# Performance work log

Hardware: AMD Instinct MI355X
Metric: run time of the kernel (lower is better)

Reference implementation:

```python
import jax, jax.numpy as jnp
import numpy as np

N_EMBD = 1024
N_HEAD = 16
HEAD_DIM = N_EMBD // N_HEAD


def setup_inputs() -> dict:
    key = jax.random.key(0)
    ks = jax.random.split(key, 8)
    B, T, T_ctx, C = 2, 2048, 2048, N_EMBD
    s = 1.0 / np.sqrt(C)
    return {
        "x": jax.random.normal(ks[0], (B, T, C), dtype=jnp.float32),
        "context": jax.random.normal(ks[1], (B, T_ctx, C), dtype=jnp.float32),
        # Linear weights stored as [in, out] (torch stores [out, in]; math identical via x @ W)
        "Wq": jax.random.normal(ks[2], (C, C), dtype=jnp.float32) * s,
        "bq": jnp.zeros((C,), dtype=jnp.float32),
        "Wkv": jax.random.normal(ks[3], (C, 2 * C), dtype=jnp.float32) * s,
        "bkv": jnp.zeros((2 * C,), dtype=jnp.float32),
        "Wp": jax.random.normal(ks[4], (C, C), dtype=jnp.float32) * s,
        "bp": jnp.zeros((C,), dtype=jnp.float32),
    }


def reference(x, context, Wq, bq, Wkv, bkv, Wp, bp):
    B, T, C = x.shape
    T_ctx = context.shape[1]
    H, D = N_HEAD, C // N_HEAD

    q = (x @ Wq + bq).reshape(B, T, H, D).transpose(0, 2, 1, 3)          # [B,H,T,D]
    kv = context @ Wkv + bkv                                             # [B,T_ctx,2C]
    k, v = jnp.split(kv, 2, axis=-1)
    k = k.reshape(B, T_ctx, H, D).transpose(0, 2, 1, 3)                  # [B,H,T_ctx,D]
    v = v.reshape(B, T_ctx, H, D).transpose(0, 2, 1, 3)                  # [B,H,T_ctx,D]

    att = jnp.einsum("bhtd,bhsd->bhts", q, k) * (1.0 / jnp.sqrt(jnp.asarray(D, q.dtype)))
    # tril(ones(T, T_ctx)): position t attends to context positions s <= t
    causal = jnp.arange(T)[:, None] >= jnp.arange(T_ctx)[None, :]        # [T,T_ctx]
    att = jnp.where(causal[None, None], att, jnp.asarray(-jnp.inf, att.dtype))
    att = jax.nn.softmax(att, axis=-1)

    y = jnp.einsum("bhts,bhsd->bhtd", att, v)                            # [B,H,T,D]
    y = y.transpose(0, 2, 1, 3).reshape(B, T, C)
    return y @ Wp + bp
```

## Files before the change

### kernel.cpp

```cpp
#include <hip/hip_runtime.h>
#include <hip/hip_bf16.h>

typedef __bf16 bf16;
typedef __bf16 bf16x8 __attribute__((ext_vector_type(8)));
typedef __bf16 bf16x4 __attribute__((ext_vector_type(4)));
typedef float f32x4 __attribute__((ext_vector_type(4)));
typedef float f32x16 __attribute__((ext_vector_type(16)));

#define GLOAD_LDS16(g, l) \
  __builtin_amdgcn_global_load_lds((const __attribute__((address_space(1))) void*)(g), \
                                   (__attribute__((address_space(3))) void*)(l), 16, 0, 0)

static __device__ __forceinline__ unsigned cvtpk_bf16(float lo, float hi) {
  unsigned r;
  asm("v_cvt_pk_bf16_f32 %0, %1, %2" : "=v"(r) : "v"(lo), "v"(hi));
  return r;
}
static __device__ __forceinline__ void pl32swap(unsigned& a, unsigned& b) {
  asm volatile("v_permlane32_swap_b32 %0, %1" : "+v"(a), "+v"(b));
}

__global__ __launch_bounds__(256) void prep_kernel(
    const float* __restrict__ x, const float* __restrict__ ctx,
    const float* __restrict__ Wq, const float* __restrict__ Wkv, const float* __restrict__ Wp,
    bf16* __restrict__ x_bf, bf16* __restrict__ c_bf,
    bf16* __restrict__ Wq_t, bf16* __restrict__ Wkv_t, bf16* __restrict__ Wp_t) {
  const int bid = blockIdx.x;
  if (bid < 8192) {
    const int i = (bid & 4095) * 256 + threadIdx.x;
    const float4 v = (bid < 4096) ? ((const float4*)x)[i] : ((const float4*)ctx)[i];
    bf16x4 o;
    o.x = (bf16)v.x; o.y = (bf16)v.y; o.z = (bf16)v.z; o.w = (bf16)v.w;
    if (bid < 4096) ((bf16x4*)x_bf)[i] = o; else ((bf16x4*)c_bf)[i] = o;
    return;
  }
  __shared__ float tile[32][33];
  int tb = bid - 8192;
  const float* W; bf16* Wt; int N;
  if (tb < 1024) { W = Wq; Wt = Wq_t; N = 1024; }
  else if (tb < 3072) { W = Wkv; Wt = Wkv_t; N = 2048; tb -= 1024; }
  else { W = Wp; Wt = Wp_t; N = 1024; tb -= 3072; }
  const int nt = N >> 5;
  const int n0 = (tb % nt) * 32, k0 = (tb / nt) * 32;
  const int tx = threadIdx.x & 31, ty = threadIdx.x >> 5;
#pragma unroll
  for (int i = 0; i < 32; i += 8)
    tile[ty + i][tx] = W[(size_t)(k0 + ty + i) * N + n0 + tx];
  __syncthreads();
#pragma unroll
  for (int i = 0; i < 32; i += 8)
    Wt[(size_t)(n0 + ty + i) * 1024 + k0 + tx] = (bf16)tile[tx][ty + i];
}

__global__ __launch_bounds__(512) void proj_gemm_kernel(
    const bf16* __restrict__ x_bf, const bf16* __restrict__ c_bf,
    const bf16* __restrict__ Wq_t, const bf16* __restrict__ Wkv_t,
    const float* __restrict__ bq, const float* __restrict__ bkv,
    bf16* __restrict__ Qh, bf16* __restrict__ Kh, bf16* __restrict__ Vt) {
  __shared__ __align__(16) bf16 SM[24576];
  bf16* As = SM;
  bf16* Bs = SM + 16384;
  bf16* Vb = SM;

  const int tid = threadIdx.x;
  const int lane = tid & 63;
  const int w = tid >> 6;
  const int wm = w >> 2, wn = w & 3;
  const int g4 = lane >> 4, r16 = lane & 15;
  const int wu = __builtin_amdgcn_readfirstlane(w);

  int bid = blockIdx.x;
  bid = (bid & 7) * 48 + (bid >> 3);
  const bool isq = bid < 128;
  const int lid = isq ? bid : bid - 128;
  const int bx = isq ? (lid & 7) : (lid & 15);
  const int by = isq ? (lid >> 3) : (lid >> 4);
  const int m0 = by * 256, n0 = bx * 128;
  const bf16* A = isq ? x_bf : c_bf;
  const bf16* Bt = isq ? Wq_t : Wkv_t;
  const float* bias = isq ? bq : bkv;

  const bf16* Abase = A + (size_t)m0 * 1024;
  const bf16* Bbase = Bt + (size_t)n0 * 1024;
  int aoff[4], boff[2];
#pragma unroll
  for (int it = 0; it < 4; ++it) {
    const int s = it * 512 + tid;
    const int row = s >> 3, j = s & 7;
    aoff[it] = row * 1024 + (j ^ (row & 7)) * 8;
  }
#pragma unroll
  for (int it = 0; it < 2; ++it) {
    const int s = it * 512 + tid;
    const int row = s >> 3, j = s & 7;
    boff[it] = row * 1024 + (j ^ (row & 7)) * 8;
  }

  f32x4 acc[8][2] = {};

  for (int k0 = 0; k0 < 1024; k0 += 64) {
    __syncthreads();
#pragma unroll
    for (int it = 0; it < 4; ++it)
      GLOAD_LDS16(Abase + aoff[it] + k0, As + (it * 512 + wu * 64) * 8);
#pragma unroll
    for (int it = 0; it < 2; ++it)
      GLOAD_LDS16(Bbase + boff[it] + k0, Bs + (it * 512 + wu * 64) * 8);
    __syncthreads();
#pragma unroll
    for (int kk = 0; kk < 2; ++kk) {
      bf16x8 bfr[2];
#pragma unroll
      for (int ni = 0; ni < 2; ni++) {
        const int lr = wn * 32 + ni * 16 + r16;
        bfr[ni] = *(const bf16x8*)(Bs + lr * 64 + ((kk * 4 + g4) ^ (lr & 7)) * 8);
      }
#pragma unroll
      for (int mi = 0; mi < 8; mi++) {
        const int lr = wm * 128 + mi * 16 + r16;
        const bf16x8 a = *(const bf16x8*)(As + lr * 64 + ((kk * 4 + g4) ^ (lr & 7)) * 8);
        acc[mi][0] = __builtin_amdgcn_mfma_f32_16x16x32_bf16(a, bfr[0], acc[mi][0], 0, 0, 0);
        acc[mi][1] = __builtin_amdgcn_mfma_f32_16x16x32_bf16(a, bfr[1], acc[mi][1], 0, 0, 0);
      }
    }
  }

  if (!isq && n0 >= 1024) {
    const int bb = m0 >> 11, t0l = m0 & 2047;
#pragma unroll
    for (int p = 0; p < 2; ++p) {
      __syncthreads();
      if ((wn >> 1) == p) {
#pragma unroll
        for (int mi = 0; mi < 8; mi++)
#pragma unroll
          for (int ni = 0; ni < 2; ni++) {
            const int cl = (wn & 1) * 32 + ni * 16 + r16;
            const float bv = bias[n0 + p * 64 + cl];
#pragma unroll
            for (int r = 0; r < 4; r++) {
              const int rl = wm * 128 + mi * 16 + 4 * g4 + r;
              Vb[cl * 264 + rl] = (bf16)(acc[mi][ni][r] + bv);
            }
          }
      }
      __syncthreads();
      const int c2b = n0 - 1024 + p * 64;
#pragma unroll
      for (int pp = 0; pp < 4; ++pp) {
        const int slot = tid + pp * 512;
        const int d = slot >> 5, j = slot & 31;
        const int cc = c2b + d;
        const int h = cc >> 6, dd = cc & 63;
        *(bf16x8*)(Vt + ((size_t)((bb * 16 + h) * 64 + dd)) * 2048 + t0l + j * 8) =
            *(const bf16x8*)(Vb + d * 264 + j * 8);
      }
    }
    return;
  }

#pragma unroll
  for (int mi = 0; mi < 8; mi++) {
#pragma unroll
    for (int ni = 0; ni < 2; ni++) {
      const int col = n0 + wn * 32 + ni * 16 + r16;
      const float bv = bias[col];
      const int rowb = m0 + wm * 128 + mi * 16 + 4 * g4;
      const int h = col >> 6, d = col & 63;
#pragma unroll
      for (int r = 0; r < 4; r++) {
        const int row = rowb + r;
        const int bb = row >> 11, t = row & 2047;
        const float v = acc[mi][ni][r] + bv;
        if (isq)
          Qh[((size_t)(bb * 16 + h) * 2048 + t) * 64 + d] = (bf16)(v * 0.18033688f);
        else
          Kh[((size_t)(bb * 16 + h) * 2048 + t) * 64 + d] = (bf16)v;
      }
    }
  }
}

__global__ __launch_bounds__(256) void gemm_out_kernel(
    const bf16* __restrict__ A, const bf16* __restrict__ Bt,
    const float* __restrict__ bias, float* __restrict__ out) {
  __shared__ __align__(16) bf16 As[128 * 64];
  __shared__ __align__(16) bf16 Bs[64 * 64];

  const int tid = threadIdx.x;
  const int lane = tid & 63;
  const int w = tid >> 6;
  const int wr = w >> 1, wc = w & 1;
  const int g4 = lane >> 4, r16 = lane & 15;
  const int wu = __builtin_amdgcn_readfirstlane(w);

  int bid = blockIdx.x;
  bid = (bid & 7) * 64 + (bid >> 3);
  const int bx = bid & 15, by = bid >> 4;
  const int m0 = by * 128, n0 = bx * 64;

  const bf16* Abase = A + (size_t)m0 * 1024;
  const bf16* Bbase = Bt + (size_t)n0 * 1024;
  int aoff[4], boff[2];
#pragma unroll
  for (int it = 0; it < 4; ++it) {
    const int s = it * 256 + tid;
    const int row = s >> 3, j = s & 7;
    aoff[it] = row * 1024 + (j ^ (row & 7)) * 8;
  }
#pragma unroll
  for (int it = 0; it < 2; ++it) {
    const int s = it * 256 + tid;
    const int row = s >> 3, j = s & 7;
    boff[it] = row * 1024 + (j ^ (row & 7)) * 8;
  }

  f32x4 acc[4][2] = {};

  for (int k0 = 0; k0 < 1024; k0 += 64) {
    __syncthreads();
#pragma unroll
    for (int it = 0; it < 4; ++it)
      GLOAD_LDS16(Abase + aoff[it] + k0, As + (it * 256 + wu * 64) * 8);
#pragma unroll
    for (int it = 0; it < 2; ++it)
      GLOAD_LDS16(Bbase + boff[it] + k0, Bs + (it * 256 + wu * 64) * 8);
    __syncthreads();
#pragma unroll
    for (int kk = 0; kk < 2; ++kk) {
      bf16x8 af[4], bfr[2];
#pragma unroll
      for (int i = 0; i < 4; i++) {
        const int lr = wr * 64 + i * 16 + r16;
        af[i] = *(const bf16x8*)(As + lr * 64 + ((kk * 4 + g4) ^ (lr & 7)) * 8);
      }
#pragma unroll
      for (int i = 0; i < 2; i++) {
        const int lr = wc * 32 + i * 16 + r16;
        bfr[i] = *(const bf16x8*)(Bs + lr * 64 + ((kk * 4 + g4) ^ (lr & 7)) * 8);
      }
#pragma unroll
      for (int mi = 0; mi < 4; mi++)
#pragma unroll
        for (int ni = 0; ni < 2; ni++)
          acc[mi][ni] = __builtin_amdgcn_mfma_f32_16x16x32_bf16(af[mi], bfr[ni], acc[mi][ni], 0, 0, 0);
    }
  }

#pragma unroll
  for (int mi = 0; mi < 4; mi++)
#pragma unroll
    for (int ni = 0; ni < 2; ni++) {
      const int col = n0 + wc * 32 + ni * 16 + r16;
      const float bv = bias[col];
      const int rowb = m0 + wr * 64 + mi * 16 + 4 * g4;
#pragma unroll
      for (int r = 0; r < 4; r++)
        out[(size_t)(rowb + r) * 1024 + col] = acc[mi][ni][r] + bv;
    }
}

#define AE2(c, tb, te, sl) ((c) | ((tb) << 3) | ((te) << 9) | ((sl) << 15))
__constant__ int ATAB[12] = {
  AE2(7, 0, 16, 6), AE2(7, 16, 32, 7), AE2(3, 0, 16, 0),
  AE2(6, 0, 14, 4), AE2(6, 14, 28, 5), AE2(5, 0, 12, 2),
  AE2(5, 12, 24, 3), AE2(2, 0, 12, 0), AE2(4, 0, 10, 0),
  AE2(4, 10, 20, 1), AE2(1, 0, 8, 0),  AE2(0, 0, 4, 0),
};

__global__ __launch_bounds__(512) void attn_kernel(
    const bf16* __restrict__ Q, const bf16* __restrict__ Kh,
    const bf16* __restrict__ Vt, bf16* __restrict__ Y,
    bf16* __restrict__ Po, float* __restrict__ Lsum) {
  __shared__ __align__(16) bf16 Kls[2][4096];
  __shared__ __align__(16) bf16 Vls[2][4096];

  const int tid = threadIdx.x;
  const int lane = tid & 63;
  const int w = tid >> 6;
  const int l31 = lane & 31;
  const int g = lane >> 5;
  const int u = blockIdx.x >> 5;
  const int bh = blockIdx.x & 31;
  const int e = ATAB[u];
  const int c = e & 7, tb = (e >> 3) & 63, te = (e >> 9) & 63, slot = (e >> 15) & 7;
  const int slotg = bh * 8 + slot;
  const bool single = (tb == 0) && (te == 4 * c + 4);
  const int b = bh >> 4, h = bh & 15;
  const int qb = c * 256;
  const int wq = qb + w * 32;
  const int wu = __builtin_amdgcn_readfirstlane(w);

  bf16x8 qf[4];
  {
    const bf16* qp = Q + ((size_t)bh * 2048 + wq + l31) * 64 + g * 8;
#pragma unroll
    for (int cc = 0; cc < 4; ++cc) qf[cc] = *(const bf16x8*)(qp + cc * 16);
  }

  f32x16 O0 = {}, O1 = {};
  float l = 0.f;

  auto stage = [&](int bi, int s0) {
    const int s = tid >> 3, j = tid & 7;
    const int js = (j ^ (s & 7)) * 8;
    GLOAD_LDS16(Kh + ((size_t)bh * 2048 + s0 + s) * 64 + js, &Kls[bi][wu * 512]);
    GLOAD_LDS16(Vt + ((size_t)bh * 64 + s) * 2048 + s0 + js, &Vls[bi][wu * 512]);
  };

  stage(tb & 1, tb * 64);

  for (int t = tb; t < te; ++t) {
    const int s0 = t * 64;
    asm volatile("s_waitcnt vmcnt(0)" ::: "memory");
    __builtin_amdgcn_s_barrier();
    asm volatile("" ::: "memory");
    if (t + 1 < te) stage((t + 1) & 1, s0 + 64);

    if (s0 < wq + 32) {
      const bf16* Kb = Kls[t & 1];
      const bf16* Vb = Vls[t & 1];

      f32x16 SA = {}, SB = {};
      __builtin_amdgcn_s_setprio(1);
#pragma unroll
      for (int cc = 0; cc < 4; ++cc) {
        const int sl = ((cc * 2 + g) ^ (l31 & 7)) * 8;
        bf16x8 kf0 = *(const bf16x8*)(Kb + l31 * 64 + sl);
        SA = __builtin_amdgcn_mfma_f32_32x32x16_bf16(kf0, qf[cc], SA, 0, 0, 0);
        bf16x8 kf1 = *(const bf16x8*)(Kb + (32 + l31) * 64 + sl);
        SB = __builtin_amdgcn_mfma_f32_32x32x16_bf16(kf1, qf[cc], SB, 0, 0, 0);
      }
      __builtin_amdgcn_s_setprio(0);

      const int qg = wq + l31;
      if (s0 + 63 > wq) {
#pragma unroll
        for (int r = 0; r < 16; ++r) {
          const int sl = (r & 3) + 8 * (r >> 2) + 4 * g;
          SA[r] = (s0 + sl <= qg) ? SA[r] : -3.0e38f;
          SB[r] = (s0 + 32 + sl <= qg) ? SB[r] : -3.0e38f;
        }
      }

      float ps = 0.f;
#pragma unroll
      for (int r = 0; r < 16; ++r) { SA[r] = __builtin_amdgcn_exp2f(SA[r]); ps += SA[r]; }
#pragma unroll
      for (int r = 0; r < 16; ++r) { SB[r] = __builtin_amdgcn_exp2f(SB[r]); ps += SB[r]; }
      l += ps;

      union PW { unsigned u[4]; bf16x8 v; };
      PW pa0, pa1, pa2, pa3;
      {
        unsigned A0 = cvtpk_bf16(SA[0], SA[1]), B0 = cvtpk_bf16(SA[2], SA[3]);
        unsigned C0 = cvtpk_bf16(SA[4], SA[5]), D0 = cvtpk_bf16(SA[6], SA[7]);
        pl32swap(A0, C0); pl32swap(B0, D0);
        pa0.u[0] = A0; pa0.u[1] = B0; pa0.u[2] = C0; pa0.u[3] = D0;

        unsigned A1 = cvtpk_bf16(SA[8], SA[9]), B1 = cvtpk_bf16(SA[10], SA[11]);
        unsigned C1 = cvtpk_bf16(SA[12], SA[13]), D1 = cvtpk_bf16(SA[14], SA[15]);
        pl32swap(A1, C1); pl32swap(B1, D1);
        pa1.u[0] = A1; pa1.u[1] = B1; pa1.u[2] = C1; pa1.u[3] = D1;

        unsigned A2 = cvtpk_bf16(SB[0], SB[1]), B2 = cvtpk_bf16(SB[2], SB[3]);
        unsigned C2 = cvtpk_bf16(SB[4], SB[5]), D2 = cvtpk_bf16(SB[6], SB[7]);
        pl32swap(A2, C2); pl32swap(B2, D2);
        pa2.u[0] = A2; pa2.u[1] = B2; pa2.u[2] = C2; pa2.u[3] = D2;

        unsigned A3 = cvtpk_bf16(SB[8], SB[9]), B3 = cvtpk_bf16(SB[10], SB[11]);
        unsigned C3 = cvtpk_bf16(SB[12], SB[13]), D3 = cvtpk_bf16(SB[14], SB[15]);
        pl32swap(A3, C3); pl32swap(B3, D3);
        pa3.u[0] = A3; pa3.u[1] = B3; pa3.u[2] = C3; pa3.u[3] = D3;
      }

      __builtin_amdgcn_s_setprio(1);
#pragma unroll
      for (int cc = 0; cc < 4; ++cc) {
        const bf16x8 pav = (cc == 0) ? pa0.v : (cc == 1) ? pa1.v : (cc == 2) ? pa2.v : pa3.v;
        const int sl = ((cc * 2 + g) ^ (l31 & 7)) * 8;
        bf16x8 vf0 = *(const bf16x8*)(Vb + l31 * 64 + sl);
        O0 = __builtin_amdgcn_mfma_f32_32x32x16_bf16(pav, vf0, O0, 0, 0, 0);
        bf16x8 vf1 = *(const bf16x8*)(Vb + (32 + l31) * 64 + sl);
        O1 = __builtin_amdgcn_mfma_f32_32x32x16_bf16(pav, vf1, O1, 0, 0, 0);
      }
      __builtin_amdgcn_s_setprio(0);
    }
  }

  l += __shfl_xor(l, 32, 64);
  if (!single && g == 0)
    Lsum[(size_t)slotg * 256 + w * 32 + l31] = l;
#pragma unroll
  for (int r = 0; r < 16; ++r) {
    const int qr = (r & 3) + 8 * (r >> 2) + (g << 2);
    const float lr = __shfl(l, qr, 64);
    const float inv = (lr > 0.f) ? 1.f / lr : 0.f;
    if (single) {
      const int tq = wq + qr;
      bf16* yp = Y + ((size_t)(b * 2048 + tq)) * 1024 + h * 64 + l31;
      yp[0]  = (bf16)(O0[r] * inv);
      yp[32] = (bf16)(O1[r] * inv);
    } else {
      bf16* pp = Po + (size_t)slotg * 16384 + (w * 32 + qr) * 64 + l31;
      pp[0]  = (bf16)(O0[r] * inv);
      pp[32] = (bf16)(O1[r] * inv);
    }
  }
}

__global__ __launch_bounds__(256) void attn_combine(
    const bf16* __restrict__ Po, const float* __restrict__ Lsum, bf16* __restrict__ Y) {
  const int bh = blockIdx.x >> 2, ci = blockIdx.x & 3;
  const int c = ci + 4;
  const int base = bh * 8 + ci * 2;
  const int b = bh >> 4, h = bh & 15;
  const int tid = threadIdx.x;
#pragma unroll
  for (int k = 0; k < 8; ++k) {
    const int tt = tid + k * 256;
    const int row = tt >> 3, cg = tt & 7;
    const float w0 = Lsum[(size_t)base * 256 + row];
    const float w1 = Lsum[(size_t)(base + 1) * 256 + row];
    const bf16x8 v0 = *(const bf16x8*)(Po + (size_t)base * 16384 + row * 64 + cg * 8);
    const bf16x8 v1 = *(const bf16x8*)(Po + (size_t)(base + 1) * 16384 + row * 64 + cg * 8);
    const float inv = 1.f / (w0 + w1);
    bf16x8 o;
#pragma unroll
    for (int j = 0; j < 8; ++j) o[j] = (bf16)((w0 * (float)v0[j] + w1 * (float)v1[j]) * inv);
    const int t = c * 256 + row;
    *(bf16x8*)(Y + ((size_t)(b * 2048 + t)) * 1024 + h * 64 + cg * 8) = o;
  }
}

extern "C" void kernel_launch(void* const* d_in, const int* in_sizes, int n_in,
                              void* d_out, int out_size, void* d_ws, size_t ws_size,
                              hipStream_t stream) {
  (void)in_sizes; (void)n_in; (void)out_size; (void)ws_size;
  const float* x   = (const float*)d_in[0];
  const float* ctx = (const float*)d_in[1];
  const float* Wq  = (const float*)d_in[2];
  const float* bq  = (const float*)d_in[3];
  const float* Wkv = (const float*)d_in[4];
  const float* bkv = (const float*)d_in[5];
  const float* Wp  = (const float*)d_in[6];
  const float* bp  = (const float*)d_in[7];
  float* out = (float*)d_out;

  char* ws = (char*)d_ws;
  const size_t MB = 1024 * 1024;
  bf16*  Po    = (bf16*)(ws + 0 * MB);
  float* Lsum  = (float*)(ws + 9 * MB);
  bf16* x_bf   = (bf16*)(ws + 0 * MB);
  bf16* c_bf   = (bf16*)(ws + 10 * MB);
  bf16* Wq_t   = (bf16*)(ws + 18 * MB);
  bf16* Wkv_t  = (bf16*)(ws + 20 * MB);
  bf16* Wp_t   = (bf16*)(ws + 24 * MB);
  bf16* Qh     = (bf16*)(ws + 26 * MB);
  bf16* Kh     = (bf16*)(ws + 34 * MB);
  bf16* Vt     = (bf16*)(ws + 42 * MB);
  bf16* y_bf   = (bf16*)(ws + 50 * MB);

  prep_kernel<<<12288, 256, 0, stream>>>(x, ctx, Wq, Wkv, Wp, x_bf, c_bf, Wq_t, Wkv_t, Wp_t);
  proj_gemm_kernel<<<384, 512, 0, stream>>>(x_bf, c_bf, Wq_t, Wkv_t, bq, bkv, Qh, Kh, Vt);
  attn_kernel<<<384, 512, 0, stream>>>(Qh, Kh, Vt, y_bf, Po, Lsum);
  attn_combine<<<128, 256, 0, stream>>>(Po, Lsum, y_bf);
  gemm_out_kernel<<<512, 256, 0, stream>>>(y_bf, Wp_t, bp, out);
}
```

Measured before the change: 97.86 us.

## Double-buffer QKV projection GEMM with BK=32 stages and prefetch

The projection GEMM's K loop changes from single-buffered 64-wide K tiles into a two-stage LDS double buffer with 32-wide K tiles. The next tile is loaded asynchronously while MFMAs run on the current one, and the swizzle is adjusted for 4-chunk rows. One barrier per iteration replaces two, and s_setprio raises priority around the MFMA block. This aims to hide global-load latency behind compute, at the cost of twice as many loop iterations, each with a full vmcnt(0) wait.

```diff
diff --git a/kernel.cpp b/kernel.cpp
--- a/kernel.cpp
+++ b/kernel.cpp
@@ -82,47 +82,59 @@
 
   const bf16* Abase = A + (size_t)m0 * 1024;
   const bf16* Bbase = Bt + (size_t)n0 * 1024;
-  int aoff[4], boff[2];
-#pragma unroll
-  for (int it = 0; it < 4; ++it) {
-    const int s = it * 512 + tid;
-    const int row = s >> 3, j = s & 7;
-    aoff[it] = row * 1024 + (j ^ (row & 7)) * 8;
-  }
+  int aoff[2], boff;
 #pragma unroll
   for (int it = 0; it < 2; ++it) {
     const int s = it * 512 + tid;
-    const int row = s >> 3, j = s & 7;
-    boff[it] = row * 1024 + (j ^ (row & 7)) * 8;
-  }
+    const int row = s >> 2, j = s & 3;
+    aoff[it] = row * 1024 + (j ^ (row & 3)) * 8;
+  }
+  {
+    const int row = tid >> 2, j = tid & 3;
+    boff = row * 1024 + (j ^ (row & 3)) * 8;
+  }
+
+  auto stage = [&](int bi, int k0) {
+    bf16* Ad = As + bi * 8192;
+    bf16* Bd = Bs + bi * 4096;
+#pragma unroll
+    for (int it = 0; it < 2; ++it)
+      GLOAD_LDS16(Abase + aoff[it] + k0, Ad + (it * 512 + wu * 64) * 8);
+    GLOAD_LDS16(Bbase + boff + k0, Bd + (wu * 64) * 8);
+  };
 
   f32x4 acc[8][2] = {};
 
-  for (int k0 = 0; k0 < 1024; k0 += 64) {
-    __syncthreads();
-#pragma unroll
-    for (int it = 0; it < 4; ++it)
-      GLOAD_LDS16(Abase + aoff[it] + k0, As + (it * 512 + wu * 64) * 8);
-#pragma unroll
-    for (int it = 0; it < 2; ++it)
-      GLOAD_LDS16(Bbase + boff[it] + k0, Bs + (it * 512 + wu * 64) * 8);
-    __syncthreads();
-#pragma unroll
-    for (int kk = 0; kk < 2; ++kk) {
-      bf16x8 bfr[2];
-#pragma unroll
-      for (int ni = 0; ni < 2; ni++) {
-        const int lr = wn * 32 + ni * 16 + r16;
-        bfr[ni] = *(const bf16x8*)(Bs + lr * 64 + ((kk * 4 + g4) ^ (lr & 7)) * 8);
-      }
-#pragma unroll
-      for (int mi = 0; mi < 8; mi++) {
-        const int lr = wm * 128 + mi * 16 + r16;
-        const bf16x8 a = *(const bf16x8*)(As + lr * 64 + ((kk * 4 + g4) ^ (lr & 7)) * 8);
-        acc[mi][0] = __builtin_amdgcn_mfma_f32_16x16x32_bf16(a, bfr[0], acc[mi][0], 0, 0, 0);
-        acc[mi][1] = __builtin_amdgcn_mfma_f32_16x16x32_bf16(a, bfr[1], acc[mi][1], 0, 0, 0);
-      }
-    }
+  stage(0, 0);
+  asm volatile("s_waitcnt vmcnt(0)" ::: "memory");
+  __builtin_amdgcn_s_barrier();
+  asm volatile("" ::: "memory");
+
+  for (int kt = 0; kt < 32; ++kt) {
+    const int bi = kt & 1;
+    if (kt + 1 < 32) stage(bi ^ 1, (kt + 1) * 32);
+
+    const bf16* Ab = As + bi * 8192;
+    const bf16* Bb = Bs + bi * 4096;
+    bf16x8 bfr[2];
+#pragma unroll
+    for (int ni = 0; ni < 2; ni++) {
+      const int lr = wn * 32 + ni * 16 + r16;
+      bfr[ni] = *(const bf16x8*)(Bb + lr * 32 + ((g4 ^ (lr & 3)) * 8));
+    }
+    __builtin_amdgcn_s_setprio(1);
+#pragma unroll
+    for (int mi = 0; mi < 8; mi++) {
+      const int lr = wm * 128 + mi * 16 + r16;
+      const bf16x8 a = *(const bf16x8*)(Ab + lr * 32 + ((g4 ^ (lr & 3)) * 8));
+      acc[mi][0] = __builtin_amdgcn_mfma_f32_16x16x32_bf16(a, bfr[0], acc[mi][0], 0, 0, 0);
+      acc[mi][1] = __builtin_amdgcn_mfma_f32_16x16x32_bf16(a, bfr[1], acc[mi][1], 0, 0, 0);
+    }
+    __builtin_amdgcn_s_setprio(0);
+
+    asm volatile("s_waitcnt vmcnt(0)" ::: "memory");
+    __builtin_amdgcn_s_barrier();
+    asm volatile("" ::: "memory");
   }
 
   if (!isq && n0 >= 1024) {
```

After: 99.61 us. Within noise of the previous version (+1.8%).
